# Kernel tuning notes

Measured on AMD Instinct MI355X. Metric: run time of the kernel, lower is better.

Reference implementation:

```python
import jax, jax.numpy as jnp
import numpy as np

PAD = 1  # deform_conv2d called with stride=1, padding=1, dilation=1 in forward


def _bilinear_gather(x, py, px):
    """Bilinear sample x [B,C,H,W] at float coords py,px [B,K,Ho,Wo].
    Out-of-bounds corners contribute zero (torchvision deform_conv2d semantics).
    Returns [B,C,K,Ho,Wo]."""
    B, C, H, W = x.shape
    y0 = jnp.floor(py)
    x0 = jnp.floor(px)
    y1, x1 = y0 + 1.0, x0 + 1.0
    wy1 = py - y0
    wy0 = 1.0 - wy1
    wx1 = px - x0
    wx0 = 1.0 - wx1
    x_flat = x.reshape(B, C, H * W)

    def corner(yi, xi, w):
        m = ((yi >= 0) & (yi < H) & (xi >= 0) & (xi < W)).astype(x.dtype)
        yc = jnp.clip(yi, 0, H - 1).astype(jnp.int32)
        xc = jnp.clip(xi, 0, W - 1).astype(jnp.int32)
        lin = (yc * W + xc).reshape(B, -1)  # [B, K*Ho*Wo]
        vals = jax.vmap(lambda xf, idx: jnp.take(xf, idx, axis=1))(x_flat, lin)
        vals = vals.reshape(B, C, *yi.shape[1:])  # [B,C,K,Ho,Wo]
        return vals * (w * m)[:, None]

    return (corner(y0, x0, wy0 * wx0) + corner(y0, x1, wy0 * wx1)
            + corner(y1, x0, wy1 * wx0) + corner(y1, x1, wy1 * wx1))


def reference(x, w_off, b_off, weight):
    B, C, H, W = x.shape
    O, Ci, kh, kw = weight.shape
    K = kh * kw
    # offset conv: Conv2d(C -> 2*k*k, kernel 3, stride 1, pad 1, groups=1)
    offset = jax.lax.conv_general_dilated(
        x, w_off, window_strides=(1, 1), padding=[(PAD, PAD), (PAD, PAD)],
        dimension_numbers=('NCHW', 'OIHW', 'NCHW')) + b_off[None, :, None, None]
    off = offset.reshape(B, K, 2, H, W)  # channel layout: (tap, [dy, dx])

    ky = jnp.repeat(jnp.arange(kh, dtype=x.dtype), kw)  # [K] kernel row index
    kx = jnp.tile(jnp.arange(kw, dtype=x.dtype), kh)    # [K] kernel col index
    ys = jnp.arange(H, dtype=x.dtype)[None, None, :, None]  # [1,1,H,1]
    xs = jnp.arange(W, dtype=x.dtype)[None, None, None, :]  # [1,1,1,W]
    py = ys + (ky - PAD)[None, :, None, None] + off[:, :, 0]  # [B,K,H,W]
    px = xs + (kx - PAD)[None, :, None, None] + off[:, :, 1]

    sampled = _bilinear_gather(x, py, px)  # [B,C,K,H,W]
    out = jnp.einsum('bckhw,ock->bohw', sampled, weight.reshape(O, Ci, K))
    return out


def setup_inputs() -> dict:
    key = jax.random.key(0)
    k1, k2, k3 = jax.random.split(key, 3)
    x = jax.random.normal(k1, (4, 64, 128, 128), dtype=jnp.float32)
    # small offset-conv weights -> modest learned offsets (realistic DCN behavior)
    w_off = jax.random.normal(k2, (18, 64, 3, 3), dtype=jnp.float32) * 0.01
    b_off = jnp.zeros((18,), dtype=jnp.float32)
    weight = jax.random.normal(k3, (64, 64, 3, 3), dtype=jnp.float32)
    return {'x': x, 'w_off': w_off, 'b_off': b_off, 'weight': weight}
```

## Files before the change

kernel.cpp:

```cpp
#include <hip/hip_runtime.h>
#include <math.h>

typedef _Float16 f16;
typedef _Float16 f16x8 __attribute__((ext_vector_type(8)));
typedef float f32x4 __attribute__((ext_vector_type(4)));

namespace {
constexpr int Bn = 4;
constexpr int Cn = 64;
constexpr int On = 64;
constexpr int Hn = 128;
constexpr int Wn = 128;
constexpr int Kn = 9;
constexpr int HWn = Hn * Wn;
constexpr int CKn = Cn * Kn;
constexpr int NPIX = Bn * HWn;
constexpr int SR = 72;
}

__global__ __launch_bounds__(256) void prep_weights(
    const float* __restrict__ w_off, const float* __restrict__ weight,
    f16* __restrict__ wofb, f16* __restrict__ wtb) {
  int t = blockIdx.x * 256 + threadIdx.x;
  if (t < Kn * On * Cn) {
    int c = t & 63, o = (t >> 6) & 63, k = t >> 12;
    wtb[t] = (f16)weight[((o << 6) + c) * 9 + k];
  }
  if (t < Kn * 32 * Cn) {
    int c = t & 63, o = (t >> 6) & 31, k = t >> 11;
    float v = (o < 18) ? w_off[((o << 6) + c) * 9 + k] : 0.f;
    wofb[t] = (f16)v;
  }
}

__global__ __launch_bounds__(256) void transpose_x(
    const float* __restrict__ x, f16* __restrict__ xt) {
  const int l = threadIdx.x & 63;
  const int cw = threadIdx.x >> 6;
  const int pixbase = blockIdx.x * 64;
  const int b = pixbase >> 14;
  const int hw = (pixbase & (HWn - 1)) + l;

  f16x8 v0, v1;
#pragma unroll
  for (int i = 0; i < 8; ++i) {
    v0[i] = (f16)x[((size_t)(b * Cn + cw * 16 + i)) * HWn + hw];
    v1[i] = (f16)x[((size_t)(b * Cn + cw * 16 + 8 + i)) * HWn + hw];
  }
  f16* dst = xt + ((size_t)(b * HWn + hw)) * 64 + cw * 16;
  *(f16x8*)dst = v0;
  *(f16x8*)(dst + 8) = v1;
}

__global__ __launch_bounds__(256) void offset_mfma(
    const f16* __restrict__ xt, const f16* __restrict__ wofb,
    const float* __restrict__ b_off, float* __restrict__ offset) {
  __shared__ __align__(16) f16 Sb[2][64 * SR];
  __shared__ __align__(16) f16 Wb[2][32 * SR];

  const int t = threadIdx.x;
  const int pixbase = blockIdx.x * 64;
  const int b = pixbase >> 14;
  const int y = (pixbase & (HWn - 1)) >> 7;
  const int xx0 = pixbase & (Wn - 1);
  const f16* xb = xt + ((size_t)b * HWn) * 64;

  const int px_s = t >> 2, cq = t & 3;
  const int lane = t & 63, wv = t >> 6;
  const int l15 = lane & 15, q = lane >> 4;
  const int m = wv & 1;
  const int nb = (wv >> 1) * 2;

  auto stage = [&](int k, int buf) {
    const int dy = k / 3 - 1, dx = k % 3 - 1;
    const int ys = y + dy, xs = xx0 + px_s + dx;
    f16* sdst = &Sb[buf][px_s * SR + cq * 16];
    if (ys >= 0 && ys < Hn && xs >= 0 && xs < Wn) {
      const f16* src = xb + (size_t)(ys * Wn + xs) * 64 + cq * 16;
      *(f16x8*)sdst = *(const f16x8*)src;
      *(f16x8*)(sdst + 8) = *(const f16x8*)(src + 8);
    } else {
      f16x8 z = {};
      *(f16x8*)sdst = z;
      *(f16x8*)(sdst + 8) = z;
    }
    const int o = t >> 3, part = t & 7;
    const f16* wsrc = wofb + (((size_t)(k * 32 + o)) << 6) + part * 8;
    *(f16x8*)&Wb[buf][o * SR + part * 8] = *(const f16x8*)wsrc;
  };

  f32x4 acc[2];
#pragma unroll
  for (int t2 = 0; t2 < 2; ++t2) acc[t2] = (f32x4){0.f, 0.f, 0.f, 0.f};

  stage(0, 0);
  __syncthreads();
  for (int k = 0; k < Kn; ++k) {
    const int cur = k & 1;
    if (k + 1 < Kn) stage(k + 1, 1 - cur);
#pragma unroll
    for (int s = 0; s < 2; ++s) {
      f16x8 af = *(const f16x8*)&Wb[cur][(m * 16 + l15) * SR + s * 32 + q * 8];
#pragma unroll
      for (int t2 = 0; t2 < 2; ++t2) {
        f16x8 bf = *(const f16x8*)
            &Sb[cur][((nb + t2) * 16 + l15) * SR + s * 32 + q * 8];
        acc[t2] = __builtin_amdgcn_mfma_f32_16x16x32_f16(af, bf, acc[t2],
                                                         0, 0, 0);
      }
    }
    __syncthreads();
  }

  float* ob = offset + ((size_t)b * HWn + y * Wn + xx0) * 18;
#pragma unroll
  for (int t2 = 0; t2 < 2; ++t2) {
#pragma unroll
    for (int r = 0; r < 4; ++r) {
      int o = m * 16 + q * 4 + r;
      if (o < 18) {
        int pxl = (nb + t2) * 16 + l15;
        ob[(size_t)pxl * 18 + o] = acc[t2][r] + b_off[o];
      }
    }
  }
}

__global__ __launch_bounds__(256, 4) void dcn_main(
    const f16* __restrict__ xt, const float* __restrict__ offset,
    const f16* __restrict__ wtb, float* __restrict__ out) {
  __shared__ __align__(16) f16 Sb[3][64 * SR];

  const int t = threadIdx.x;
  const int px_s = t >> 2, cq = t & 3;
  const int pxg = blockIdx.x * 64 + px_s;
  const int b = pxg >> 14;
  const int rem = pxg & (HWn - 1);
  const int y = rem >> 7;
  const int xx = rem & (Wn - 1);
  const f16* xb = xt + (((size_t)b) << 14) * 64;

  const int lane = t & 63, wv = t >> 6;
  const int l15 = lane & 15, q = lane >> 4;
  const int obase = wv * 16;

  float2 off9[9];
  {
    const float* ofp = offset + (size_t)pxg * 18;
#pragma unroll
    for (int k = 0; k < Kn; ++k) off9[k] = *(const float2*)(ofp + 2 * k);
  }

  f32x4 acc[4];
#pragma unroll
  for (int pt = 0; pt < 4; ++pt) acc[pt] = (f32x4){0.f, 0.f, 0.f, 0.f};

  for (int g = 0; g < 3; ++g) {
    if (g) __syncthreads();

    f16x8 wf[3][2];
#pragma unroll
    for (int j = 0; j < 3; ++j)
#pragma unroll
      for (int s = 0; s < 2; ++s)
        wf[j][s] = *(const f16x8*)(wtb +
            (((size_t)((3 * g + j) * 64 + obase + l15)) << 6) + s * 32 + q * 8);

#pragma unroll
    for (int j = 0; j < 3; ++j) {
      const int k = 3 * g + j;
      const int dy = k / 3 - 1, dx = k % 3 - 1;
      float py = (float)(y + dy) + off9[k].x;
      float pxf = (float)(xx + dx) + off9[k].y;
      float y0f = floorf(py), x0f = floorf(pxf);
      int y0 = (int)y0f, x0 = (int)x0f;
      int y1 = y0 + 1, x1 = x0 + 1;
      float wy1 = py - y0f, wx1 = pxf - x0f;
      float wy0 = 1.f - wy1, wx0 = 1.f - wx1;
      float my0 = (y0 >= 0 && y0 < Hn) ? 1.f : 0.f;
      float my1 = (y1 >= 0 && y1 < Hn) ? 1.f : 0.f;
      float mx0 = (x0 >= 0 && x0 < Wn) ? 1.f : 0.f;
      float mx1 = (x1 >= 0 && x1 < Wn) ? 1.f : 0.f;
      f16 h00 = (f16)(wy0 * wx0 * my0 * mx0);
      f16 h01 = (f16)(wy0 * wx1 * my0 * mx1);
      f16 h10 = (f16)(wy1 * wx0 * my1 * mx0);
      f16 h11 = (f16)(wy1 * wx1 * my1 * mx1);
      int cy0 = min(max(y0, 0), Hn - 1), cy1 = min(max(y1, 0), Hn - 1);
      int cx0 = min(max(x0, 0), Wn - 1), cx1 = min(max(x1, 0), Wn - 1);
      const f16* r00 = xb + (size_t)(cy0 * Wn + cx0) * 64 + cq * 16;
      const f16* r01 = xb + (size_t)(cy0 * Wn + cx1) * 64 + cq * 16;
      const f16* r10 = xb + (size_t)(cy1 * Wn + cx0) * 64 + cq * 16;
      const f16* r11 = xb + (size_t)(cy1 * Wn + cx1) * 64 + cq * 16;
      f16* sdst = &Sb[j][px_s * SR + cq * 16];
#pragma unroll
      for (int h = 0; h < 2; ++h) {
        f16x8 a = *(const f16x8*)(r00 + h * 8);
        f16x8 b2 = *(const f16x8*)(r01 + h * 8);
        f16x8 c = *(const f16x8*)(r10 + h * 8);
        f16x8 d = *(const f16x8*)(r11 + h * 8);
        f16x8 v = a * h00 + b2 * h01 + c * h10 + d * h11;
        *(f16x8*)(sdst + h * 8) = v;
      }
    }
    __syncthreads();

#pragma unroll
    for (int j = 0; j < 3; ++j)
#pragma unroll
      for (int s = 0; s < 2; ++s)
#pragma unroll
        for (int pt = 0; pt < 4; ++pt) {
          f16x8 bf =
              *(const f16x8*)&Sb[j][(pt * 16 + l15) * SR + s * 32 + q * 8];
          acc[pt] = __builtin_amdgcn_mfma_f32_16x16x32_f16(wf[j][s], bf,
                                                           acc[pt], 0, 0, 0);
        }
  }

  const int hw0 = (blockIdx.x * 64) & (HWn - 1);
  const int bb = (blockIdx.x * 64) >> 14;
  float* ob = out + (size_t)bb * On * HWn + hw0;
#pragma unroll
  for (int pt = 0; pt < 4; ++pt) {
#pragma unroll
    for (int r = 0; r < 4; ++r) {
      int o = obase + q * 4 + r;
      ob[(size_t)o * HWn + pt * 16 + l15] = acc[pt][r];
    }
  }
}

extern "C" void kernel_launch(void* const* d_in, const int* in_sizes, int n_in,
                              void* d_out, int out_size, void* d_ws, size_t ws_size,
                              hipStream_t stream) {
  const float* x = (const float*)d_in[0];
  const float* w_off = (const float*)d_in[1];
  const float* b_off = (const float*)d_in[2];
  const float* weight = (const float*)d_in[3];
  float* out = (float*)d_out;

  f16* xt = (f16*)d_ws;
  float* offset = (float*)(xt + (size_t)NPIX * Cn);
  f16* wtb = (f16*)(offset + (size_t)NPIX * 18);
  f16* wofb = wtb + Kn * On * Cn;

  prep_weights<<<dim3(144), dim3(256), 0, stream>>>(w_off, weight, wofb, wtb);
  transpose_x<<<dim3(NPIX / 64), dim3(256), 0, stream>>>(x, xt);
  offset_mfma<<<dim3(NPIX / 64), dim3(256), 0, stream>>>(xt, wofb, b_off,
                                                         offset);
  dcn_main<<<dim3(NPIX / 64), dim3(256), 0, stream>>>(xt, offset, wtb, out);
}
```

Baseline: 112.7 us.

## Fuse offset convolution into deformable conv kernel via shared-memory offsets

Merges the offset-conv MFMA kernel into the main deformable-conv kernel. Each block first computes its 64 pixels' 18 offsets into LDS, reusing the 3-slot sample buffer and 3-tap grouping, then runs the bilinear gather and main GEMM. This removes one launch and the global write and read of the offset tensor. In exchange it drops the original double-buffered staging, loads offset weights straight from global into registers, and adds an LDS array that may affect occupancy.

```diff
diff --git a/kernel.cpp b/kernel.cpp
--- a/kernel.cpp
+++ b/kernel.cpp
@@ -52,104 +52,94 @@
   *(f16x8*)(dst + 8) = v1;
 }
 
-__global__ __launch_bounds__(256) void offset_mfma(
+__global__ __launch_bounds__(256, 4) void dcn_fused(
     const f16* __restrict__ xt, const f16* __restrict__ wofb,
-    const float* __restrict__ b_off, float* __restrict__ offset) {
-  __shared__ __align__(16) f16 Sb[2][64 * SR];
-  __shared__ __align__(16) f16 Wb[2][32 * SR];
+    const f16* __restrict__ wtb, const float* __restrict__ b_off,
+    float* __restrict__ out) {
+  __shared__ __align__(16) f16 Sb[3][64 * SR];
+  __shared__ float off_lds[64][20];
 
   const int t = threadIdx.x;
+  const int px_s = t >> 2, cq = t & 3;
   const int pixbase = blockIdx.x * 64;
   const int b = pixbase >> 14;
   const int y = (pixbase & (HWn - 1)) >> 7;
   const int xx0 = pixbase & (Wn - 1);
+  const int xx = xx0 + px_s;
   const f16* xb = xt + ((size_t)b * HWn) * 64;
 
-  const int px_s = t >> 2, cq = t & 3;
   const int lane = t & 63, wv = t >> 6;
   const int l15 = lane & 15, q = lane >> 4;
-  const int m = wv & 1;
-  const int nb = (wv >> 1) * 2;
-
-  auto stage = [&](int k, int buf) {
-    const int dy = k / 3 - 1, dx = k % 3 - 1;
-    const int ys = y + dy, xs = xx0 + px_s + dx;
-    f16* sdst = &Sb[buf][px_s * SR + cq * 16];
-    if (ys >= 0 && ys < Hn && xs >= 0 && xs < Wn) {
-      const f16* src = xb + (size_t)(ys * Wn + xs) * 64 + cq * 16;
-      *(f16x8*)sdst = *(const f16x8*)src;
-      *(f16x8*)(sdst + 8) = *(const f16x8*)(src + 8);
-    } else {
-      f16x8 z = {};
-      *(f16x8*)sdst = z;
-      *(f16x8*)(sdst + 8) = z;
+
+  {
+    const int mA = wv & 1;
+    const int nbA = (wv >> 1) * 2;
+    f32x4 accA[2];
+#pragma unroll
+    for (int t2 = 0; t2 < 2; ++t2) accA[t2] = (f32x4){0.f, 0.f, 0.f, 0.f};
+
+    for (int g = 0; g < 3; ++g) {
+      if (g) __syncthreads();
+
+      f16x8 wfA[3][2];
+#pragma unroll
+      for (int j = 0; j < 3; ++j)
+#pragma unroll
+        for (int s = 0; s < 2; ++s)
+          wfA[j][s] = *(const f16x8*)(wofb +
+              (((size_t)((3 * g + j) * 32 + mA * 16 + l15)) << 6) +
+              s * 32 + q * 8);
+
+#pragma unroll
+      for (int j = 0; j < 3; ++j) {
+        const int k = 3 * g + j;
+        const int dy = k / 3 - 1, dx = k % 3 - 1;
+        const int ys = y + dy, xs = xx + dx;
+        f16* sdst = &Sb[j][px_s * SR + cq * 16];
+        if (ys >= 0 && ys < Hn && xs >= 0 && xs < Wn) {
+          const f16* src = xb + (size_t)(ys * Wn + xs) * 64 + cq * 16;
+          *(f16x8*)sdst = *(const f16x8*)src;
+          *(f16x8*)(sdst + 8) = *(const f16x8*)(src + 8);
+        } else {
+          f16x8 z = {};
+          *(f16x8*)sdst = z;
+          *(f16x8*)(sdst + 8) = z;
+        }
+      }
+      __syncthreads();
+
+#pragma unroll
+      for (int j = 0; j < 3; ++j)
+#pragma unroll
+        for (int s = 0; s < 2; ++s)
+#pragma unroll
+          for (int t2 = 0; t2 < 2; ++t2) {
+            f16x8 bf = *(const f16x8*)
+                &Sb[j][((nbA + t2) * 16 + l15) * SR + s * 32 + q * 8];
+            accA[t2] = __builtin_amdgcn_mfma_f32_16x16x32_f16(wfA[j][s], bf,
+                                                              accA[t2],
+                                                              0, 0, 0);
+          }
     }
-    const int o = t >> 3, part = t & 7;
-    const f16* wsrc = wofb + (((size_t)(k * 32 + o)) << 6) + part * 8;
-    *(f16x8*)&Wb[buf][o * SR + part * 8] = *(const f16x8*)wsrc;
-  };
-
-  f32x4 acc[2];
-#pragma unroll
-  for (int t2 = 0; t2 < 2; ++t2) acc[t2] = (f32x4){0.f, 0.f, 0.f, 0.f};
-
-  stage(0, 0);
-  __syncthreads();
-  for (int k = 0; k < Kn; ++k) {
-    const int cur = k & 1;
-    if (k + 1 < Kn) stage(k + 1, 1 - cur);
-#pragma unroll
-    for (int s = 0; s < 2; ++s) {
-      f16x8 af = *(const f16x8*)&Wb[cur][(m * 16 + l15) * SR + s * 32 + q * 8];
-#pragma unroll
-      for (int t2 = 0; t2 < 2; ++t2) {
-        f16x8 bf = *(const f16x8*)
-            &Sb[cur][((nb + t2) * 16 + l15) * SR + s * 32 + q * 8];
-        acc[t2] = __builtin_amdgcn_mfma_f32_16x16x32_f16(af, bf, acc[t2],
-                                                         0, 0, 0);
+
+#pragma unroll
+    for (int t2 = 0; t2 < 2; ++t2)
+#pragma unroll
+      for (int r = 0; r < 4; ++r) {
+        int o = mA * 16 + q * 4 + r;
+        if (o < 18) {
+          int pxl = (nbA + t2) * 16 + l15;
+          off_lds[pxl][o] = accA[t2][r] + b_off[o];
+        }
       }
-    }
     __syncthreads();
   }
 
-  float* ob = offset + ((size_t)b * HWn + y * Wn + xx0) * 18;
-#pragma unroll
-  for (int t2 = 0; t2 < 2; ++t2) {
-#pragma unroll
-    for (int r = 0; r < 4; ++r) {
-      int o = m * 16 + q * 4 + r;
-      if (o < 18) {
-        int pxl = (nb + t2) * 16 + l15;
-        ob[(size_t)pxl * 18 + o] = acc[t2][r] + b_off[o];
-      }
-    }
-  }
-}
-
-__global__ __launch_bounds__(256, 4) void dcn_main(
-    const f16* __restrict__ xt, const float* __restrict__ offset,
-    const f16* __restrict__ wtb, float* __restrict__ out) {
-  __shared__ __align__(16) f16 Sb[3][64 * SR];
-
-  const int t = threadIdx.x;
-  const int px_s = t >> 2, cq = t & 3;
-  const int pxg = blockIdx.x * 64 + px_s;
-  const int b = pxg >> 14;
-  const int rem = pxg & (HWn - 1);
-  const int y = rem >> 7;
-  const int xx = rem & (Wn - 1);
-  const f16* xb = xt + (((size_t)b) << 14) * 64;
-
-  const int lane = t & 63, wv = t >> 6;
-  const int l15 = lane & 15, q = lane >> 4;
   const int obase = wv * 16;
-
   float2 off9[9];
-  {
-    const float* ofp = offset + (size_t)pxg * 18;
-#pragma unroll
-    for (int k = 0; k < Kn; ++k) off9[k] = *(const float2*)(ofp + 2 * k);
-  }
+#pragma unroll
+  for (int k = 0; k < Kn; ++k)
+    off9[k] = *(const float2*)&off_lds[px_s][2 * k];
 
   f32x4 acc[4];
 #pragma unroll
@@ -217,9 +207,7 @@
         }
   }
 
-  const int hw0 = (blockIdx.x * 64) & (HWn - 1);
-  const int bb = (blockIdx.x * 64) >> 14;
-  float* ob = out + (size_t)bb * On * HWn + hw0;
+  float* ob = out + (size_t)b * On * HWn + (y * Wn + xx0);
 #pragma unroll
   for (int pt = 0; pt < 4; ++pt) {
 #pragma unroll
@@ -240,13 +228,11 @@
   float* out = (float*)d_out;
 
   f16* xt = (f16*)d_ws;
-  float* offset = (float*)(xt + (size_t)NPIX * Cn);
-  f16* wtb = (f16*)(offset + (size_t)NPIX * 18);
+  f16* wtb = xt + (size_t)NPIX * Cn;
   f16* wofb = wtb + Kn * On * Cn;
 
   prep_weights<<<dim3(144), dim3(256), 0, stream>>>(w_off, weight, wofb, wtb);
   transpose_x<<<dim3(NPIX / 64), dim3(256), 0, stream>>>(x, xt);
-  offset_mfma<<<dim3(NPIX / 64), dim3(256), 0, stream>>>(xt, wofb, b_off,
-                                                         offset);
-  dcn_main<<<dim3(NPIX / 64), dim3(256), 0, stream>>>(xt, offset, wtb, out);
-}
+  dcn_fused<<<dim3(NPIX / 64), dim3(256), 0, stream>>>(xt, wofb, wtb, b_off,
+                                                       out);
+}
```

New measurement: 113.4 us. About the same (+0.7%).
